# Optimization experiments

Measured on AMD Instinct MI355X. Metric: run time of the kernel, lower is better.

## Reference

```python
import jax, jax.numpy as jnp
import numpy as np

COST_CLASS, COST_BBOX, COST_GIOU = 1.0, 5.0, 2.0


def _box_area(b):
    return (b[..., 2] - b[..., 0]) * (b[..., 3] - b[..., 1])


def _generalized_box_iou(b1, b2):
    # b1: (B,Q,4), b2: (B,N,4), xyxy -> (B,Q,N)
    a1 = _box_area(b1)[:, :, None]
    a2 = _box_area(b2)[:, None, :]
    lt = jnp.maximum(b1[:, :, None, :2], b2[:, None, :, :2])
    rb = jnp.minimum(b1[:, :, None, 2:], b2[:, None, :, 2:])
    wh = jnp.clip(rb - lt, 0.0)
    inter = wh[..., 0] * wh[..., 1]
    union = a1 + a2 - inter
    iou = inter / union
    lt_c = jnp.minimum(b1[:, :, None, :2], b2[:, None, :, :2])
    rb_c = jnp.maximum(b1[:, :, None, 2:], b2[:, None, :, 2:])
    wh_c = jnp.clip(rb_c - lt_c, 0.0)
    area_c = wh_c[..., 0] * wh_c[..., 1]
    return iou - (area_c - union) / area_c


@jax.jit
def _cost_matrix(pred_logits, pred_boxes, tgt_labels, tgt_boxes):
    B, Q, _ = pred_logits.shape
    N = tgt_labels.shape[1]
    out_prob = jax.nn.softmax(pred_logits, axis=-1)  # (B,Q,C+1)
    idx = jnp.broadcast_to(tgt_labels[:, None, :], (B, Q, N))
    cost_class = -jnp.take_along_axis(out_prob, idx, axis=-1)          # (B,Q,N)
    cost_bbox = jnp.abs(pred_boxes[:, :, None, :] - tgt_boxes[:, None, :, :]).sum(-1)  # L1 cdist
    cost_giou = -_generalized_box_iou(pred_boxes, tgt_boxes)
    return COST_CLASS * cost_class + COST_BBOX * cost_bbox + COST_GIOU * cost_giou


def _lsa(cost):
    """Shortest-augmenting-path Hungarian (Jonker-Volgenant style).
    cost: (n, m) with n <= m. Returns col4row[i] = assigned column of row i.
    Matches scipy.optimize.linear_sum_assignment (minimization)."""
    n, m = cost.shape
    INF = np.inf
    u = np.zeros(n + 1)
    v = np.zeros(m + 1)
    p = np.zeros(m + 1, dtype=np.int64)   # p[j] = row (1-indexed) assigned to col j
    way = np.zeros(m + 1, dtype=np.int64)
    for i in range(1, n + 1):
        p[0] = i
        j0 = 0
        minv = np.full(m + 1, INF)
        used = np.zeros(m + 1, dtype=bool)
        while True:
            used[j0] = True
            i0 = p[j0]
            cur = cost[i0 - 1] - u[i0] - v[1:]
            free = ~used[1:]
            upd = free & (cur < minv[1:])
            minv[1:][upd] = cur[upd]
            way[1:][upd] = j0
            cand = np.where(free, minv[1:], INF)
            j1 = int(np.argmin(cand)) + 1
            delta = cand[j1 - 1]
            uj = np.nonzero(used)[0]
            u[p[uj]] += delta
            v[uj] -= delta
            minv[~used] -= delta
            j0 = j1
            if p[j0] == 0:
                break
        while j0 != 0:
            j1 = way[j0]
            p[j0] = p[j1]
            j0 = j1
    col4row = np.zeros(n, dtype=np.int64)
    for j in range(1, m + 1):
        if p[j] != 0:
            col4row[p[j] - 1] = j - 1
    return col4row


def setup_inputs() -> dict:
    key = jax.random.key(0)
    k1, k2, k3, k4, k5 = jax.random.split(key, 5)
    B, Q, N, C1 = 64, 600, 80, 92

    def make_boxes(kx, ky, shape):
        xy = jax.random.uniform(kx, shape + (2,)) * 0.6
        wh = jax.random.uniform(ky, shape + (2,)) * 0.35 + 0.02
        return jnp.concatenate([xy, xy + wh], axis=-1)  # valid xyxy

    pred_logits = jax.random.normal(k1, (B, Q, C1), dtype=jnp.float32)
    pred_boxes = make_boxes(k2, k3, (B, Q))
    tgt_labels = jax.random.randint(k4, (B, N), 0, 91)
    tgt_boxes = make_boxes(k5, jax.random.fold_in(k5, 1), (B, N))
    return {"pred_logits": pred_logits, "pred_boxes": pred_boxes,
            "tgt_labels": tgt_labels, "tgt_boxes": tgt_boxes}


def reference(pred_logits, pred_boxes, tgt_labels, tgt_boxes):
    # Batched cost-matrix build on device, then host Hungarian per sample
    # (mirrors the original's .cpu().numpy() + scipy linear_sum_assignment).
    C = np.asarray(_cost_matrix(pred_logits, pred_boxes, tgt_labels, tgt_boxes))  # (B,Q,N)
    B, Q, N = C.shape
    rows = np.empty((B, N), dtype=np.int64)
    cols = np.empty((B, N), dtype=np.int64)
    for b in range(B):
        q_of_t = _lsa(C[b].T)              # transpose: N <= Q; query index per target
        order = np.argsort(q_of_t, kind="stable")
        rows[b] = q_of_t[order]            # sorted query (row) indices
        cols[b] = order                    # matching target (col) indices
    return jnp.asarray(rows), jnp.asarray(cols)
```

## Files before the change

### kernel.cpp

```cpp
#include <hip/hip_runtime.h>
#include <math.h>

#define BB 64
#define QQ 600
#define NT 80
#define NC 92
#define SLOTS 10
#define NTILE 10
#define NTHR 256
#define NWAVE 4
#define MAXROUNDS 16
#define STALLCAP 3
#define SPINCAP (1 << 20)
#define MAGIC 0x5A17C0DE


template <int CTRL>
__device__ __forceinline__ int dppi(int x) {
    return __builtin_amdgcn_update_dpp(x, x, CTRL, 0xF, 0xF, false);
}

__device__ __forceinline__ unsigned wave_min_u32(unsigned x) {
    unsigned y;
    y = (unsigned)dppi<0x121>((int)x); x = x < y ? x : y;
    y = (unsigned)dppi<0x122>((int)x); x = x < y ? x : y;
    y = (unsigned)dppi<0x124>((int)x); x = x < y ? x : y;
    y = (unsigned)dppi<0x128>((int)x); x = x < y ? x : y;
    y = (unsigned)__builtin_amdgcn_ds_swizzle((int)x, 0x401F); x = x < y ? x : y;
    y = (unsigned)__shfl_xor((int)x, 32); x = x < y ? x : y;
    return x;
}

__device__ __forceinline__ unsigned long long wave_min_key64(
        unsigned long long key, int* winlane) {
    const unsigned hi = (unsigned)(key >> 32), lo = (unsigned)key;
    const unsigned mhi = wave_min_u32(hi);
    unsigned long long t = __ballot(hi == mhi);
    unsigned mlo;
    if (__popcll(t) > 1) {
        mlo = wave_min_u32((hi == mhi) ? lo : 0xFFFFFFFFu);
        t = __ballot(hi == mhi && lo == mlo);
    } else {
        mlo = (unsigned)__shfl((int)lo, __builtin_ctzll(t));
    }
    *winlane = __builtin_ctzll(t);
    return ((unsigned long long)mhi << 32) | mlo;
}

__device__ __forceinline__ unsigned long long wave_min_key64_val(
        unsigned long long key) {
    const unsigned hi = (unsigned)(key >> 32), lo = (unsigned)key;
    const unsigned mhi = wave_min_u32(hi);
    const unsigned long long t = __ballot(hi == mhi);
    unsigned mlo;
    if (__popcll(t) > 1) mlo = wave_min_u32((hi == mhi) ? lo : 0xFFFFFFFFu);
    else                 mlo = (unsigned)__shfl((int)lo, __builtin_ctzll(t));
    return ((unsigned long long)mhi << 32) | mlo;
}

__device__ __forceinline__ unsigned f32_key(float f) {
    unsigned b = __float_as_uint(f);
    return b ^ ((unsigned)((int)b >> 31) | 0x80000000u);
}
__device__ __forceinline__ float key_f32(unsigned k) {
    unsigned b = (k & 0x80000000u) ? (k ^ 0x80000000u) : ~k;
    return __uint_as_float(b);
}
__device__ __forceinline__ unsigned long long f64_key(double d) {
    unsigned long long b = (unsigned long long)__double_as_longlong(d);
    return b ^ ((unsigned long long)((long long)b >> 63) | 0x8000000000000000ULL);
}
__device__ __forceinline__ double key_f64(unsigned long long k) {
    unsigned long long b = (k & 0x8000000000000000ULL) ? (k ^ 0x8000000000000000ULL) : ~k;
    return __longlong_as_double((long long)b);
}

__global__ __launch_bounds__(256) void matcher_kernel(
    const float* __restrict__ logits,
    const float* __restrict__ pboxes,
    const int*   __restrict__ tlabels,
    const float* __restrict__ tboxes,
    float* __restrict__ cost,
    float* __restrict__ pm1,
    float* __restrict__ pm2,
    int*   __restrict__ pmj,
    int*   __restrict__ done,
    int* __restrict__ rows_out,
    int* __restrict__ cols_out)
{
    __shared__ float tile[64 * 93];
    __shared__ float s_pm[4 * 64], s_ps[4 * 64];
    __shared__ float s_tb[NT * 4];
    __shared__ int   s_tl[NT];
    __shared__ double vA[QQ];
    __shared__ double u[NT];
    __shared__ double bidm1[NT], bidm2[NT];
    __shared__ int    bidj[NT], bidver[NT];
    __shared__ int    pA[QQ];
    __shared__ int    verA[QQ];
    __shared__ int    colrow[QQ];
    __shared__ int    assigned[NT];
    __shared__ int    plist[NT];
    __shared__ int    pcnt;
    __shared__ int    wayA[QQ];
    __shared__ int    c4r[NT];
    __shared__ int    djkA[NT];

    const int g   = blockIdx.x;
    const int b   = g / NTILE;
    const int tix = g % NTILE;
    const int tid = threadIdx.x;
    const int qq  = tid & 63;
    const int wv  = tid >> 6;
    const float* C = cost + (size_t)b * NT * QQ;

    {
        const int q0 = tix * 64;
        const int nq = min(64, QQ - q0);
        const float* src = logits + ((size_t)b * QQ + q0) * NC;
        for (int idx = tid; idx < nq * NC; idx += 256) {
            const int r = idx / NC;
            tile[r * 93 + (idx - r * NC)] = src[idx];
        }
        for (int i = tid; i < NT * 4; i += 256) s_tb[i] = tboxes[b * NT * 4 + i];
        for (int i = tid; i < NT;     i += 256) s_tl[i] = tlabels[b * NT + i];
        __syncthreads();

        {
            const int c0 = wv * 23;
            const float* r = &tile[qq * 93];
            float pm = r[c0];
            #pragma unroll 11
            for (int c = 1; c < 23; ++c) pm = fmaxf(pm, r[c0 + c]);
            s_pm[wv * 64 + qq] = pm;
        }
        __syncthreads();
        {
            const int c0 = wv * 23;
            float* r = &tile[qq * 93];
            const float m = fmaxf(fmaxf(s_pm[qq], s_pm[64 + qq]),
                                  fmaxf(s_pm[128 + qq], s_pm[192 + qq]));
            float sum = 0.f;
            #pragma unroll 11
            for (int c = 0; c < 23; ++c) {
                const float e = expf(r[c0 + c] - m);
                r[c0 + c] = e;
                sum += e;
            }
            s_ps[wv * 64 + qq] = sum;
        }
        __syncthreads();

        const bool valid = qq < nq;
        float px1 = 0.f, py1 = 0.f, px2 = 0.f, py2 = 0.f, pa = 0.f, inv_s = 1.f;
        if (valid) {
            const float* pb = pboxes + ((size_t)b * QQ + q0 + qq) * 4;
            px1 = pb[0]; py1 = pb[1]; px2 = pb[2]; py2 = pb[3];
            pa  = (px2 - px1) * (py2 - py1);
            const float s = (s_ps[qq] + s_ps[64 + qq]) + (s_ps[128 + qq] + s_ps[192 + qq]);
            inv_s = 1.f / s;
        }
        float* crow = cost + (size_t)b * NT * QQ + q0 + qq;

        for (int tt = 0; tt < 20; ++tt) {
            const int t = wv * 20 + tt;
            float costv = INFINITY;
            if (valid) {
                const int lbl = s_tl[t];
                const float cc = -(tile[qq * 93 + lbl] * inv_s);
                const float tx1 = s_tb[t*4+0], ty1 = s_tb[t*4+1];
                const float tx2 = s_tb[t*4+2], ty2 = s_tb[t*4+3];
                const float cb = fabsf(px1-tx1) + fabsf(py1-ty1)
                               + fabsf(px2-tx2) + fabsf(py2-ty2);
                const float ta = (tx2 - tx1) * (ty2 - ty1);
                const float iw = fmaxf(fminf(px2, tx2) - fmaxf(px1, tx1), 0.f);
                const float ih = fmaxf(fminf(py2, ty2) - fmaxf(py1, ty1), 0.f);
                const float inter = iw * ih;
                const float uni   = pa + ta - inter;
                const float iou   = inter / uni;
                const float cw = fmaxf(fmaxf(px2, tx2) - fminf(px1, tx1), 0.f);
                const float ch = fmaxf(fmaxf(py2, ty2) - fminf(py1, ty1), 0.f);
                const float ac = cw * ch;
                const float giou = iou - (ac - uni) / ac;
                costv = (1.0f * cc + 5.0f * cb) + 2.0f * (-giou);
                crow[(size_t)t * QQ] = costv;
            }
            const unsigned key  = f32_key(costv);
            const unsigned kmin = wave_min_u32(key);
            const unsigned long long tied = __ballot(key == kmin);
            const int winlane = __builtin_ctzll(tied);
            const unsigned cand = (qq == winlane) ? 0xFFFFFFFFu : key;
            const unsigned k2   = wave_min_u32(cand);
            if (qq == 0) {
                const size_t idx = ((size_t)b * NT + t) * NTILE + tix;
                pm1[idx] = key_f32(kmin); pm2[idx] = key_f32(k2);
                pmj[idx] = q0 + winlane;
            }
        }
    }
    __syncthreads();
    if (tid == 0)
        __hip_atomic_store(&done[b * 16 + tix], MAGIC, __ATOMIC_RELEASE, __HIP_MEMORY_SCOPE_AGENT);
    if (tix != 0) return;

    if (tid < NTILE) {
        int spins = 0;
        while (__hip_atomic_load(&done[b * 16 + tid], __ATOMIC_ACQUIRE, __HIP_MEMORY_SCOPE_AGENT) != MAGIC) {
            __builtin_amdgcn_s_sleep(8);
            if (++spins > SPINCAP) break;
        }
    }
    __syncthreads();

    for (int c = tid; c < QQ; c += NTHR) { pA[c] = -1; verA[c] = 0; vA[c] = 0.0; }
    if (tid < NT) { assigned[tid] = 0; bidver[tid] = 0; }
    __syncthreads();

    if (tid < NT) {
        const int t = tid;
        const float* p1 = pm1 + ((size_t)b * NT + t) * NTILE;
        const float* p2 = pm2 + ((size_t)b * NT + t) * NTILE;
        const int*   pj = pmj + ((size_t)b * NT + t) * NTILE;
        float m1 = INFINITY, m2 = INFINITY; int j1 = QQ;
        for (int k = 0; k < NTILE; ++k) {
            const float a1 = p1[k], a2 = p2[k];
            const int   aj = pj[k];
            if (a1 < m1) { m2 = fminf(m1, a2); m1 = a1; j1 = aj; }
            else         { m2 = fminf(m2, a1); }
        }
        bidm1[t] = (double)m1; bidm2[t] = (double)m2; bidj[t] = j1;
        u[t] = (double)m1;
    }
    __syncthreads();

    int prev_np = 0x7fffffff, stall = 0;
    for (int round = 0; round < MAXROUNDS; ++round) {
        for (int c = tid; c < QQ; c += NTHR) colrow[c] = 0x7fffffff;
        if (tid == 0) pcnt = 0;
        __syncthreads();
        if (tid < NT && !assigned[tid]) {
            const int j = bidj[tid];
            if (bidver[tid] == verA[j]) atomicMin(&colrow[j], tid);
        }
        __syncthreads();
        if (tid < NT && !assigned[tid]) {
            const int i = tid, j = bidj[i];
            if (bidver[i] == verA[j] && colrow[j] == i) {
                const double m1 = bidm1[i], m2 = bidm2[i];
                const int prev = pA[j];
                pA[j] = i;
                verA[j] = verA[j] + 1;
                vA[j] -= (m2 - m1);
                u[i] = m2;
                assigned[i] = 1;
                if (prev >= 0) assigned[prev] = 0;
            }
        }
        __syncthreads();
        if (tid < NT && !assigned[tid]) { const int k = atomicAdd(&pcnt, 1); plist[k] = tid; }
        __syncthreads();
        const int np = pcnt;
        if (np == 0) break;
        if (np >= prev_np) { if (++stall >= STALLCAP) break; }
        else               { stall = 0; }
        prev_np = np;
        for (int idx = wv; idx < np; idx += NWAVE) {
            const int i = plist[idx];
            const float* rp = C + (size_t)i * QQ;
            float rowv[SLOTS];
            #pragma unroll
            for (int k = 0; k < SLOTS; ++k) { const int c = qq + 64*k; rowv[k] = (c < QQ) ? rp[c] : 0.f; }
            double m1 = INFINITY, m2 = INFINITY; int j1 = QQ;
            #pragma unroll
            for (int k = 0; k < SLOTS; ++k) {
                const int c = qq + 64 * k;
                if (c < QQ) {
                    const double key = (double)rowv[k] - vA[c];
                    if (key < m1)      { m2 = m1; m1 = key; j1 = c; }
                    else if (key < m2) { m2 = key; }
                }
            }
            int winlane;
            const unsigned long long kminv = wave_min_key64(f64_key(m1), &winlane);
            const unsigned long long c2 = (qq == winlane) ? f64_key(m2) : f64_key(m1);
            const unsigned long long k2minv = wave_min_key64_val(c2);
            const int jwin = __shfl(j1, winlane);
            if (qq == 0) {
                bidm1[i] = key_f64(kminv); bidm2[i] = key_f64(k2minv); bidj[i] = jwin;
                bidver[i] = verA[jwin];
                u[i] = key_f64(kminv);
            }
        }
        __syncthreads();
    }

    if (wv != 0) return;
    const int lane = qq;

    int nd = 0;
    for (int i = 0; i < NT; ++i) {
        if (!assigned[i]) { if (lane == 0) djkA[nd] = i; ++nd; }
    }

    double v_[SLOTS], minv_[SLOTS];
    int p_[SLOTS];
    #pragma unroll
    for (int k = 0; k < SLOTS; ++k) {
        const int c = lane + 64 * k;
        v_[k] = (c < QQ) ? vA[c] : 0.0;
        p_[k] = (c < QQ) ? pA[c] : -1;
    }

    float rowv[SLOTS];
    for (int ii = 0; ii < nd; ++ii) {
        const int i = djkA[ii];
        #pragma unroll
        for (int k = 0; k < SLOTS; ++k) minv_[k] = INFINITY;
        unsigned usedm = 0;
        int j0 = -1;
        double ui0 = u[i];
        {
            const float* rp = C + (size_t)i * QQ;
            #pragma unroll
            for (int k = 0; k < SLOTS; ++k) { const int c = lane + 64*k; rowv[k] = (c < QQ) ? rp[c] : 0.f; }
        }
        int j1, i1;

        for (;;) {
            if (j0 >= 0 && (j0 & 63) == lane) usedm |= 1u << (j0 >> 6);

            double bestv = INFINITY; int bestc = QQ;
            #pragma unroll
            for (int k = 0; k < SLOTS; ++k) {
                const int c = lane + 64 * k;
                if (c < QQ && !((usedm >> k) & 1u)) {
                    const double cur = ((double)rowv[k] - ui0) - v_[k];
                    if (cur < minv_[k]) { minv_[k] = cur; wayA[c] = j0; }
                    if (minv_[k] < bestv) { bestv = minv_[k]; bestc = c; }
                }
            }
            int winlane;
            const unsigned long long kminv = wave_min_key64(f64_key(bestv), &winlane);
            const double delta = key_f64(kminv);
            j1 = __shfl(bestc, winlane);

            {
                const int slot = j1 >> 6, lj = j1 & 63;
                int myp = p_[0];
                #pragma unroll
                for (int k = 1; k < SLOTS; ++k) if (slot == k) myp = p_[k];
                i1 = __shfl(myp, lj);
            }

            double ui_next = 0.0;
            float rown[SLOTS];
            if (i1 >= 0) {
                ui_next = u[i1];
                const float* rp = C + (size_t)i1 * QQ;
                #pragma unroll
                for (int k = 0; k < SLOTS; ++k) { const int c = lane + 64*k; rown[k] = (c < QQ) ? rp[c] : 0.f; }
            }

            #pragma unroll
            for (int k = 0; k < SLOTS; ++k) {
                const int c = lane + 64 * k;
                if (c < QQ) {
                    if ((usedm >> k) & 1u) { v_[k] -= delta; u[p_[k]] += delta; }
                    else                     minv_[k] -= delta;
                }
            }
            if (lane == 0) u[i] += delta;

            j0 = j1;
            if (i1 < 0) break;
            ui0 = ui_next;
            #pragma unroll
            for (int k = 0; k < SLOTS; ++k) rowv[k] = rown[k];
        }

        if (lane == 0) {
            int jj = j1;
            while (jj >= 0) {
                const int pr = wayA[jj];
                pA[jj] = (pr < 0) ? i : pA[pr];
                jj = pr;
            }
        }
        #pragma unroll
        for (int k = 0; k < SLOTS; ++k) {
            const int c = lane + 64 * k;
            p_[k] = (c < QQ) ? pA[c] : -1;
        }
    }

    #pragma unroll
    for (int k = 0; k < SLOTS; ++k) {
        const int c = lane + 64 * k;
        if (c < QQ) { const int t = pA[c]; if (t >= 0) c4r[t] = c; }
    }
    for (int t = lane; t < NT; t += 64) {
        const int c = c4r[t];
        int rank = 0;
        for (int t2 = 0; t2 < NT; ++t2) rank += (c4r[t2] < c) ? 1 : 0;
        rows_out[b * NT + rank] = c;
        cols_out[b * NT + rank] = t;
    }
}

extern "C" void kernel_launch(void* const* d_in, const int* in_sizes, int n_in,
                              void* d_out, int out_size, void* d_ws, size_t ws_size,
                              hipStream_t stream) {
    (void)in_sizes; (void)n_in; (void)out_size; (void)ws_size;
    const float* logits  = (const float*)d_in[0];
    const float* pboxes  = (const float*)d_in[1];
    const int*   tlabels = (const int*)d_in[2];
    const float* tboxes  = (const float*)d_in[3];
    float* cost = (float*)d_ws;
    float* pm1  = cost + (size_t)BB * NT * QQ;
    float* pm2  = pm1  + (size_t)BB * NT * NTILE;
    int*   pmj  = (int*)(pm2 + (size_t)BB * NT * NTILE);
    int*   done = pmj + (size_t)BB * NT * NTILE;
    int*   out  = (int*)d_out;

    matcher_kernel<<<dim3(BB * NTILE), NTHR, 0, stream>>>(
        logits, pboxes, tlabels, tboxes, cost, pm1, pm2, pmj, done,
        out, out + BB * NT);
}
```

Measured before the change: 119.9 us.

## Split fused matcher into cost-build and solver kernels instead of spin-wait

Replaces the single fused kernel, where tile-0 blocks spin on atomic done-flags waiting for sibling tiles, with two launches: a cost/partial-min kernel over all tiles and a separate per-batch Hungarian solver kernel. This removes the inter-block spin synchronization and the shared-memory footprint of both phases living in one kernel, which could raise occupancy of each phase. It adds a second kernel launch and forces the solver to start only after all cost tiles finish, losing the overlap where early batches could begin solving.

Measured after the change: 108.1 us, median of 2. 9.8% less time.

```diff
diff --git a/kernel.cpp b/kernel.cpp
--- a/kernel.cpp
+++ b/kernel.cpp
@@ -11,8 +11,6 @@
 #define NWAVE 4
 #define MAXROUNDS 16
 #define STALLCAP 3
-#define SPINCAP (1 << 20)
-#define MAGIC 0x5A17C0DE
 
 
 template <int CTRL>
@@ -75,7 +73,7 @@
     return __longlong_as_double((long long)b);
 }
 
-__global__ __launch_bounds__(256) void matcher_kernel(
+__global__ __launch_bounds__(256) void phasea_kernel(
     const float* __restrict__ logits,
     const float* __restrict__ pboxes,
     const int*   __restrict__ tlabels,
@@ -83,15 +81,112 @@
     float* __restrict__ cost,
     float* __restrict__ pm1,
     float* __restrict__ pm2,
-    int*   __restrict__ pmj,
-    int*   __restrict__ done,
-    int* __restrict__ rows_out,
-    int* __restrict__ cols_out)
+    int*   __restrict__ pmj)
 {
     __shared__ float tile[64 * 93];
     __shared__ float s_pm[4 * 64], s_ps[4 * 64];
     __shared__ float s_tb[NT * 4];
     __shared__ int   s_tl[NT];
+
+    const int g   = blockIdx.x;
+    const int b   = g / NTILE;
+    const int tix = g % NTILE;
+    const int tid = threadIdx.x;
+    const int qq  = tid & 63;
+    const int wv  = tid >> 6;
+
+    const int q0 = tix * 64;
+    const int nq = min(64, QQ - q0);
+    const float* src = logits + ((size_t)b * QQ + q0) * NC;
+    for (int idx = tid; idx < nq * NC; idx += 256) {
+        const int r = idx / NC;
+        tile[r * 93 + (idx - r * NC)] = src[idx];
+    }
+    for (int i = tid; i < NT * 4; i += 256) s_tb[i] = tboxes[b * NT * 4 + i];
+    for (int i = tid; i < NT;     i += 256) s_tl[i] = tlabels[b * NT + i];
+    __syncthreads();
+
+    {
+        const int c0 = wv * 23;
+        const float* r = &tile[qq * 93];
+        float pm = r[c0];
+        #pragma unroll 11
+        for (int c = 1; c < 23; ++c) pm = fmaxf(pm, r[c0 + c]);
+        s_pm[wv * 64 + qq] = pm;
+    }
+    __syncthreads();
+    {
+        const int c0 = wv * 23;
+        float* r = &tile[qq * 93];
+        const float m = fmaxf(fmaxf(s_pm[qq], s_pm[64 + qq]),
+                              fmaxf(s_pm[128 + qq], s_pm[192 + qq]));
+        float sum = 0.f;
+        #pragma unroll 11
+        for (int c = 0; c < 23; ++c) {
+            const float e = expf(r[c0 + c] - m);
+            r[c0 + c] = e;
+            sum += e;
+        }
+        s_ps[wv * 64 + qq] = sum;
+    }
+    __syncthreads();
+
+    const bool valid = qq < nq;
+    float px1 = 0.f, py1 = 0.f, px2 = 0.f, py2 = 0.f, pa = 0.f, inv_s = 1.f;
+    if (valid) {
+        const float* pb = pboxes + ((size_t)b * QQ + q0 + qq) * 4;
+        px1 = pb[0]; py1 = pb[1]; px2 = pb[2]; py2 = pb[3];
+        pa  = (px2 - px1) * (py2 - py1);
+        const float s = (s_ps[qq] + s_ps[64 + qq]) + (s_ps[128 + qq] + s_ps[192 + qq]);
+        inv_s = 1.f / s;
+    }
+    float* crow = cost + (size_t)b * NT * QQ + q0 + qq;
+
+    for (int tt = 0; tt < 20; ++tt) {
+        const int t = wv * 20 + tt;
+        float costv = INFINITY;
+        if (valid) {
+            const int lbl = s_tl[t];
+            const float cc = -(tile[qq * 93 + lbl] * inv_s);
+            const float tx1 = s_tb[t*4+0], ty1 = s_tb[t*4+1];
+            const float tx2 = s_tb[t*4+2], ty2 = s_tb[t*4+3];
+            const float cb = fabsf(px1-tx1) + fabsf(py1-ty1)
+                           + fabsf(px2-tx2) + fabsf(py2-ty2);
+            const float ta = (tx2 - tx1) * (ty2 - ty1);
+            const float iw = fmaxf(fminf(px2, tx2) - fmaxf(px1, tx1), 0.f);
+            const float ih = fmaxf(fminf(py2, ty2) - fmaxf(py1, ty1), 0.f);
+            const float inter = iw * ih;
+            const float uni   = pa + ta - inter;
+            const float iou   = inter / uni;
+            const float cw = fmaxf(fmaxf(px2, tx2) - fminf(px1, tx1), 0.f);
+            const float ch = fmaxf(fmaxf(py2, ty2) - fminf(py1, ty1), 0.f);
+            const float ac = cw * ch;
+            const float giou = iou - (ac - uni) / ac;
+            costv = (1.0f * cc + 5.0f * cb) + 2.0f * (-giou);
+            crow[(size_t)t * QQ] = costv;
+        }
+        const unsigned key  = f32_key(costv);
+        const unsigned kmin = wave_min_u32(key);
+        const unsigned long long tied = __ballot(key == kmin);
+        const int winlane = __builtin_ctzll(tied);
+        const unsigned cand = (qq == winlane) ? 0xFFFFFFFFu : key;
+        const unsigned k2   = wave_min_u32(cand);
+        if (qq == 0) {
+            const size_t idx = ((size_t)b * NT + t) * NTILE + tix;
+            pm1[idx] = key_f32(kmin); pm2[idx] = key_f32(k2);
+            pmj[idx] = q0 + winlane;
+        }
+    }
+}
+
+__global__ __launch_bounds__(256) void solver_kernel(
+    const float* __restrict__ cost,
+    const float* __restrict__ pm1,
+    const float* __restrict__ pm2,
+    const int*   __restrict__ pmj,
+    int* __restrict__ rows_out,
+    int* __restrict__ cols_out)
+{
     __shared__ double vA[QQ];
     __shared__ double u[NT];
     __shared__ double bidm1[NT], bidm2[NT];
@@ -106,111 +201,11 @@
     __shared__ int    c4r[NT];
     __shared__ int    djkA[NT];
 
-    const int g   = blockIdx.x;
-    const int b   = g / NTILE;
-    const int tix = g % NTILE;
+    const int b   = blockIdx.x;
     const int tid = threadIdx.x;
     const int qq  = tid & 63;
     const int wv  = tid >> 6;
     const float* C = cost + (size_t)b * NT * QQ;
-
-    {
-        const int q0 = tix * 64;
-        const int nq = min(64, QQ - q0);
-        const float* src = logits + ((size_t)b * QQ + q0) * NC;
-        for (int idx = tid; idx < nq * NC; idx += 256) {
-            const int r = idx / NC;
-            tile[r * 93 + (idx - r * NC)] = src[idx];
-        }
-        for (int i = tid; i < NT * 4; i += 256) s_tb[i] = tboxes[b * NT * 4 + i];
-        for (int i = tid; i < NT;     i += 256) s_tl[i] = tlabels[b * NT + i];
-        __syncthreads();
-
-        {
-            const int c0 = wv * 23;
-            const float* r = &tile[qq * 93];
-            float pm = r[c0];
-            #pragma unroll 11
-            for (int c = 1; c < 23; ++c) pm = fmaxf(pm, r[c0 + c]);
-            s_pm[wv * 64 + qq] = pm;
-        }
-        __syncthreads();
-        {
-            const int c0 = wv * 23;
-            float* r = &tile[qq * 93];
-            const float m = fmaxf(fmaxf(s_pm[qq], s_pm[64 + qq]),
-                                  fmaxf(s_pm[128 + qq], s_pm[192 + qq]));
-            float sum = 0.f;
-            #pragma unroll 11
-            for (int c = 0; c < 23; ++c) {
-                const float e = expf(r[c0 + c] - m);
-                r[c0 + c] = e;
-                sum += e;
-            }
-            s_ps[wv * 64 + qq] = sum;
-        }
-        __syncthreads();
-
-        const bool valid = qq < nq;
-        float px1 = 0.f, py1 = 0.f, px2 = 0.f, py2 = 0.f, pa = 0.f, inv_s = 1.f;
-        if (valid) {
-            const float* pb = pboxes + ((size_t)b * QQ + q0 + qq) * 4;
-            px1 = pb[0]; py1 = pb[1]; px2 = pb[2]; py2 = pb[3];
-            pa  = (px2 - px1) * (py2 - py1);
-            const float s = (s_ps[qq] + s_ps[64 + qq]) + (s_ps[128 + qq] + s_ps[192 + qq]);
-            inv_s = 1.f / s;
-        }
-        float* crow = cost + (size_t)b * NT * QQ + q0 + qq;
-
-        for (int tt = 0; tt < 20; ++tt) {
-            const int t = wv * 20 + tt;
-            float costv = INFINITY;
-            if (valid) {
-                const int lbl = s_tl[t];
-                const float cc = -(tile[qq * 93 + lbl] * inv_s);
-                const float tx1 = s_tb[t*4+0], ty1 = s_tb[t*4+1];
-                const float tx2 = s_tb[t*4+2], ty2 = s_tb[t*4+3];
-                const float cb = fabsf(px1-tx1) + fabsf(py1-ty1)
-                               + fabsf(px2-tx2) + fabsf(py2-ty2);
-                const float ta = (tx2 - tx1) * (ty2 - ty1);
-                const float iw = fmaxf(fminf(px2, tx2) - fmaxf(px1, tx1), 0.f);
-                const float ih = fmaxf(fminf(py2, ty2) - fmaxf(py1, ty1), 0.f);
-                const float inter = iw * ih;
-                const float uni   = pa + ta - inter;
-                const float iou   = inter / uni;
-                const float cw = fmaxf(fmaxf(px2, tx2) - fminf(px1, tx1), 0.f);
-                const float ch = fmaxf(fmaxf(py2, ty2) - fminf(py1, ty1), 0.f);
-                const float ac = cw * ch;
-                const float giou = iou - (ac - uni) / ac;
-                costv = (1.0f * cc + 5.0f * cb) + 2.0f * (-giou);
-                crow[(size_t)t * QQ] = costv;
-            }
-            const unsigned key  = f32_key(costv);
-            const unsigned kmin = wave_min_u32(key);
-            const unsigned long long tied = __ballot(key == kmin);
-            const int winlane = __builtin_ctzll(tied);
-            const unsigned cand = (qq == winlane) ? 0xFFFFFFFFu : key;
-            const unsigned k2   = wave_min_u32(cand);
-            if (qq == 0) {
-                const size_t idx = ((size_t)b * NT + t) * NTILE + tix;
-                pm1[idx] = key_f32(kmin); pm2[idx] = key_f32(k2);
-                pmj[idx] = q0 + winlane;
-            }
-        }
-    }
-    __syncthreads();
-    if (tid == 0)
-        __hip_atomic_store(&done[b * 16 + tix], MAGIC, __ATOMIC_RELEASE, __HIP_MEMORY_SCOPE_AGENT);
-    if (tix != 0) return;
-
-    if (tid < NTILE) {
-        int spins = 0;
-        while (__hip_atomic_load(&done[b * 16 + tid], __ATOMIC_ACQUIRE, __HIP_MEMORY_SCOPE_AGENT) != MAGIC) {
-            __builtin_amdgcn_s_sleep(8);
-            if (++spins > SPINCAP) break;
-        }
-    }
-    __syncthreads();
 
     for (int c = tid; c < QQ; c += NTHR) { pA[c] = -1; verA[c] = 0; vA[c] = 0.0; }
     if (tid < NT) { assigned[tid] = 0; bidver[tid] = 0; }
@@ -419,10 +414,10 @@
     float* pm1  = cost + (size_t)BB * NT * QQ;
     float* pm2  = pm1  + (size_t)BB * NT * NTILE;
     int*   pmj  = (int*)(pm2 + (size_t)BB * NT * NTILE);
-    int*   done = pmj + (size_t)BB * NT * NTILE;
     int*   out  = (int*)d_out;
 
-    matcher_kernel<<<dim3(BB * NTILE), NTHR, 0, stream>>>(
-        logits, pboxes, tlabels, tboxes, cost, pm1, pm2, pmj, done,
-        out, out + BB * NT);
-}
+    phasea_kernel<<<dim3(BB * NTILE), NTHR, 0, stream>>>(
+        logits, pboxes, tlabels, tboxes, cost, pm1, pm2, pmj);
+    solver_kernel<<<dim3(BB), NTHR, 0, stream>>>(
+        cost, pm1, pm2, pmj, out, out + BB * NT);
+}
```
